# Performance work log

Hardware: AMD Instinct MI355X
Metric: run time of the kernel (lower is better)

The kernel has to match this reference:

```python
import jax, jax.numpy as jnp
import numpy as np
import math

B, T, C, H = 2, 2048, 512, 8
K, DIL = 3, 1
EPS = 1e-5


def _ln(x, g, b):
    m = jnp.mean(x, axis=-1, keepdims=True)
    v = jnp.mean(jnp.square(x - m), axis=-1, keepdims=True)
    return (x - m) * jax.lax.rsqrt(v + EPS) * g + b


def setup_inputs() -> dict:
    key = jax.random.key(0)
    ks = jax.random.split(key, 12)
    s = 0.02
    return {
        "x": jax.random.normal(ks[0], (B, T, C), jnp.float32),
        "conv_w": jax.random.normal(ks[1], (C, C, K), jnp.float32) * s,  # OIH
        "conv_b": jax.random.normal(ks[2], (C,), jnp.float32) * s,
        "g1": jnp.ones((C,), jnp.float32), "b1": jnp.zeros((C,), jnp.float32),
        "qkv_w": jax.random.normal(ks[3], (C, 3 * C), jnp.float32) * s,
        "qkv_b": jax.random.normal(ks[4], (3 * C,), jnp.float32) * s,
        "proj_w": jax.random.normal(ks[5], (C, C), jnp.float32) * s,
        "proj_b": jax.random.normal(ks[6], (C,), jnp.float32) * s,
        "g2": jnp.ones((C,), jnp.float32), "b2": jnp.zeros((C,), jnp.float32),
        "ffn_w1": jax.random.normal(ks[7], (C, 2 * C), jnp.float32) * s,
        "ffn_b1": jax.random.normal(ks[8], (2 * C,), jnp.float32) * s,
        "ffn_w2": jax.random.normal(ks[9], (2 * C, C), jnp.float32) * s,
        "ffn_b2": jax.random.normal(ks[10], (C,), jnp.float32) * s,
        "g3": jnp.ones((C,), jnp.float32), "b3": jnp.zeros((C,), jnp.float32),
    }


def reference(x, conv_w, conv_b, g1, b1, qkv_w, qkv_b, proj_w, proj_b,
              g2, b2, ffn_w1, ffn_b1, ffn_w2, ffn_b2, g3, b3):
    b, t, c = x.shape
    hd = c // H
    # --- causal dilated conv (left-pad only == pad both + right-trim) ---
    pad = (K - 1) * DIL
    xc = jnp.transpose(x, (0, 2, 1))  # [B,C,T]
    conv = jax.lax.conv_general_dilated(
        xc, conv_w, window_strides=(1,), padding=[(pad, 0)],
        rhs_dilation=(DIL,), dimension_numbers=("NCH", "OIH", "NCH"))
    conv = conv + conv_b[None, :, None]
    x = _ln(x + jnp.transpose(conv, (0, 2, 1)), g1, b1)
    # --- causal self-attention ---
    qkv = (x @ qkv_w + qkv_b).reshape(b, t, 3, H, hd)
    qkv = jnp.transpose(qkv, (2, 0, 3, 1, 4))  # [3,B,H,T,hd]
    q, k, v = qkv[0], qkv[1], qkv[2]
    scores = jnp.einsum("bhqd,bhkd->bhqk", q, k) / math.sqrt(hd)
    causal = jnp.tril(jnp.ones((t, t), bool))
    scores = jnp.where(causal, scores, -jnp.inf)
    attn = jax.nn.softmax(scores, axis=-1)
    out = jnp.einsum("bhqk,bhkd->bhqd", attn, v)
    out = jnp.transpose(out, (0, 2, 1, 3)).reshape(b, t, c)
    out = out @ proj_w + proj_b
    x = _ln(x + out, g2, b2)
    # --- FFN ---
    ffn = jax.nn.relu(x @ ffn_w1 + ffn_b1) @ ffn_w2 + ffn_b2
    return _ln(x + ffn, g3, b3)
```

## Files before the change

### kernel.cpp

```cpp
#include <hip/hip_runtime.h>
#include <hip/hip_bf16.h>

#define TT 2048

typedef __attribute__((ext_vector_type(4))) float f32x4;
typedef __attribute__((ext_vector_type(8))) __bf16 bf16x8;
typedef __attribute__((ext_vector_type(4))) short short4v;

enum { M_CONV = 0, M_QKV = 1, M_PROJ = 2, M_FFN1 = 3, M_FFN2 = 4 };

__device__ __forceinline__ void gload16(const void* g, void* l) {
    __builtin_amdgcn_global_load_lds(
        (__attribute__((address_space(1))) void*)g,
        (__attribute__((address_space(3))) void*)l, 16, 0, 0);
}

__device__ __forceinline__ short f2bf(float f) {
    unsigned u = __float_as_uint(f);
    u = (u + 0x7fffu + ((u >> 16) & 1u)) >> 16;
    return (short)u;
}

__global__ void cast_all(const float* __restrict__ conv_w, const float* __restrict__ x,
                         short* __restrict__ cwT, short* __restrict__ xpad) {
    int idx = blockIdx.x * 256 + threadIdx.x;
    if (idx < 786432) {
        int tap = idx >> 18, i = (idx >> 9) & 511, o = idx & 511;
        cwT[(size_t)o * 1536 + tap * 512 + i] = f2bf(conv_w[((size_t)o * 512 + i) * 3 + tap]);
        return;
    }
    idx -= 786432;
    if (idx < 2099200) {
        int i = idx & 511, rp = idx >> 9;
        int bb = rp / 2050, rr = rp - bb * 2050;
        int t = rr - 2;
        float v = (t >= 0) ? x[((size_t)(bb << 11) + t) * 512 + i] : 0.f;
        xpad[((size_t)bb * 2050 + rr) * 512 + i] = f2bf(v);
    }
}

__global__ __launch_bounds__(256) void transpose_cast(
    const float* __restrict__ qkv_w, const float* __restrict__ proj_w,
    const float* __restrict__ f1w, const float* __restrict__ f2w,
    short* __restrict__ qkvT, short* __restrict__ projT,
    short* __restrict__ f1T, short* __restrict__ f2T) {
    int t = blockIdx.x;
    const float* src; short* dst; int K, N, lt;
    if (t < 768)       { src = qkv_w;  dst = qkvT;  K = 512;  N = 1536; lt = t; }
    else if (t < 1024) { src = proj_w; dst = projT; K = 512;  N = 512;  lt = t - 768; }
    else if (t < 1536) { src = f1w;    dst = f1T;   K = 512;  N = 1024; lt = t - 1024; }
    else               { src = f2w;    dst = f2T;   K = 1024; N = 512;  lt = t - 1536; }
    int ntn = N >> 5;
    int kt = lt / ntn, nt = lt - kt * ntn;
    int k0 = kt * 32, n0 = nt * 32;
    __shared__ float tile[32][33];
    int c = threadIdx.x & 31, r = threadIdx.x >> 5;
    #pragma unroll
    for (int i = 0; i < 4; i++)
        tile[r + i * 8][c] = src[(size_t)(k0 + r + i * 8) * N + n0 + c];
    __syncthreads();
    #pragma unroll
    for (int i = 0; i < 4; i++)
        dst[(size_t)(n0 + r + i * 8) * K + k0 + c] = f2bf(tile[c][r + i * 8]);
}

__global__ __launch_bounds__(512) void ln_row(const float* __restrict__ in,
                                              const float* __restrict__ g,
                                              const float* __restrict__ b,
                                              float* __restrict__ outf,
                                              short* __restrict__ outb) {
    int row = blockIdx.x * 8 + (threadIdx.x >> 6);
    int l = threadIdx.x & 63;
    const float* p = in + (size_t)row * 512 + l * 8;
    f32x4 v0 = *(const f32x4*)p;
    f32x4 v1 = *(const f32x4*)(p + 4);
    float s = 0.f, ss = 0.f;
    #pragma unroll
    for (int i = 0; i < 4; i++) { s += v0[i]; ss += v0[i] * v0[i]; }
    #pragma unroll
    for (int i = 0; i < 4; i++) { s += v1[i]; ss += v1[i] * v1[i]; }
    #pragma unroll
    for (int off = 1; off < 64; off <<= 1) {
        s  += __shfl_xor(s, off);
        ss += __shfl_xor(ss, off);
    }
    float mean = s * (1.f / 512);
    float var  = ss * (1.f / 512) - mean * mean;
    float rstd = rsqrtf(var + 1e-5f);
    f32x4 g0 = *(const f32x4*)(g + l * 8), g1 = *(const f32x4*)(g + l * 8 + 4);
    f32x4 b0 = *(const f32x4*)(b + l * 8), b1 = *(const f32x4*)(b + l * 8 + 4);
    f32x4 o0, o1;
    #pragma unroll
    for (int i = 0; i < 4; i++) {
        o0[i] = (v0[i] - mean) * rstd * g0[i] + b0[i];
        o1[i] = (v1[i] - mean) * rstd * g1[i] + b1[i];
    }
    float* q = outf + (size_t)row * 512 + l * 8;
    *(f32x4*)q = o0;
    *(f32x4*)(q + 4) = o1;
    if (outb) {
        short4v p0, p1;
        #pragma unroll
        for (int i = 0; i < 4; i++) { p0[i] = f2bf(o0[i]); p1[i] = f2bf(o1[i]); }
        *(short4v*)(outb + (size_t)row * 512 + l * 8) = p0;
        *(short4v*)(outb + (size_t)row * 512 + l * 8 + 4) = p1;
    }
}

template<int MODE>
__device__ __forceinline__ const short* a_ptr(const short* A, int m0, int r, int kk, int K) {
    if constexpr (MODE == M_CONV) {
        int row = m0 + r;
        int bb = row >> 11, t5 = row & 2047;
        int tap = kk >> 9, k2 = kk & 511;
        return A + ((size_t)(bb * 2050 + t5 + tap) * 512 + k2);
    } else {
        return A + ((size_t)(m0 + r) * K + kk);
    }
}

template<int MODE>
__global__ __launch_bounds__(256) void gemm_mfma(
    const short* __restrict__ A, const short* __restrict__ Bw,
    const float* __restrict__ bias, const float* __restrict__ res,
    void* __restrict__ Cout, short* __restrict__ vTb, int K) {
    __shared__ short As[64 * 64];
    __shared__ short Bs[64 * 64];
    const int tid = threadIdx.x;
    const int w = tid >> 6, l = tid & 63;
    const int wm = w >> 1, wn = w & 1;
    const int lr = l & 15, lc = l >> 4;
    const int m0 = blockIdx.x * 64, n0 = blockIdx.y * 64;
    f32x4 acc[2][2];
    #pragma unroll
    for (int mf = 0; mf < 2; mf++)
        #pragma unroll
        for (int nf = 0; nf < 2; nf++) acc[mf][nf] = (f32x4){0.f, 0.f, 0.f, 0.f};

    for (int k0 = 0; k0 < K; k0 += 64) {
        #pragma unroll
        for (int i = 0; i < 2; i++) {
            int u = i * 256 + tid;
            int r = u >> 3, c = (u & 7) ^ (r & 7);
            gload16(a_ptr<MODE>(A, m0, r, k0 + c * 8, K), (char*)As + u * 16);
            gload16(Bw + ((size_t)(n0 + r) * K + k0 + c * 8), (char*)Bs + u * 16);
        }
        __syncthreads();
        bf16x8 af[2][2], bfv[2][2];
        #pragma unroll
        for (int mf = 0; mf < 2; mf++)
            #pragma unroll
            for (int ks = 0; ks < 2; ks++) {
                int rr = wm * 32 + mf * 16 + lr;
                int cc = (ks * 4 + lc) ^ (rr & 7);
                af[mf][ks] = *(const bf16x8*)&As[rr * 64 + cc * 8];
            }
        #pragma unroll
        for (int nf = 0; nf < 2; nf++)
            #pragma unroll
            for (int ks = 0; ks < 2; ks++) {
                int rr = wn * 32 + nf * 16 + lr;
                int cc = (ks * 4 + lc) ^ (rr & 7);
                bfv[nf][ks] = *(const bf16x8*)&Bs[rr * 64 + cc * 8];
            }
        __builtin_amdgcn_s_setprio(1);
        #pragma unroll
        for (int nf = 0; nf < 2; nf++)
            #pragma unroll
            for (int ks = 0; ks < 2; ks++)
                #pragma unroll
                for (int mf = 0; mf < 2; mf++)
                    acc[mf][nf] = __builtin_amdgcn_mfma_f32_16x16x32_bf16(
                        af[mf][ks], bfv[nf][ks], acc[mf][nf], 0, 0, 0);
        __builtin_amdgcn_s_setprio(0);
        __syncthreads();
    }
    #pragma unroll
    for (int mf = 0; mf < 2; mf++) {
        int row0 = m0 + wm * 32 + mf * 16 + lc * 4;
        #pragma unroll
        for (int nf = 0; nf < 2; nf++) {
            int col = n0 + wn * 32 + nf * 16 + lr;
            float bv = bias[col];
            if constexpr (MODE == M_CONV || MODE == M_PROJ || MODE == M_FFN2) {
                float* Cf = (float*)Cout;
                #pragma unroll
                for (int rg = 0; rg < 4; rg++) {
                    size_t off = (size_t)(row0 + rg) * 512 + col;
                    Cf[off] = acc[mf][nf][rg] + bv + res[off];
                }
            } else if constexpr (MODE == M_FFN1) {
                short* Cb = (short*)Cout;
                #pragma unroll
                for (int rg = 0; rg < 4; rg++)
                    Cb[(size_t)(row0 + rg) * 1024 + col] =
                        f2bf(fmaxf(acc[mf][nf][rg] + bv, 0.f));
            } else {
                short* Cb = (short*)Cout;
                float v[4];
                #pragma unroll
                for (int rg = 0; rg < 4; rg++) {
                    v[rg] = acc[mf][nf][rg] + bv;
                    Cb[(size_t)(row0 + rg) * 1536 + col] = f2bf(v[rg]);
                }
                if (col >= 1024) {
                    int vc = col - 1024, hh = vc >> 6, dd = vc & 63;
                    int bb = row0 >> 11, t5 = row0 & 2047;
                    short4v pk = {f2bf(v[0]), f2bf(v[1]), f2bf(v[2]), f2bf(v[3])};
                    *(short4v*)&vTb[((size_t)((bb << 3) + hh) * 64 + dd) * 2048 + t5] = pk;
                }
            }
        }
    }
}

__global__ __launch_bounds__(512) void attn_mfma(const short* __restrict__ qkvb,
                                                 const short* __restrict__ vTb,
                                                 short* __restrict__ aout) {
    __shared__ short SM[25600];
    __shared__ float Mm[4][16], Lm[4][16];
    const int tid = threadIdx.x;
    const int w = tid >> 6, l = tid & 63;
    const int half = w >> 2, wq = w & 3;
    const int lr = l & 15, lc = l >> 4;
    const int L = blockIdx.x;
    const int bh = L & 15;
    const int qt = 31 - (L >> 4);
    const int b = bh >> 3, h = bh & 7;
    const int qr = wq * 16, q0 = qt * 64;
    const int pbase = 16384 + w * (16 * 72);

    {
        int u = tid, r = u >> 3, c = (u & 7) ^ (r & 7);
        gload16(qkvb + ((size_t)(b * 2048 + q0 + r) * 1536 + h * 64 + c * 8),
                (char*)&SM[16384] + u * 16);
    }
    __syncthreads();
    bf16x8 aq[2];
    #pragma unroll
    for (int ks = 0; ks < 2; ks++) {
        int rr = qr + lr;
        int cc = (lc + 4 * ks) ^ (rr & 7);
        aq[ks] = *(const bf16x8*)&SM[16384 + rr * 64 + cc * 8];
    }
    __syncthreads();

    f32x4 o[4];
    float mst[4], lst[4];
    #pragma unroll
    for (int nf = 0; nf < 4; nf++) o[nf] = (f32x4){0.f, 0.f, 0.f, 0.f};
    #pragma unroll
    for (int rg = 0; rg < 4; rg++) { mst[rg] = -1e30f; lst[rg] = 0.f; }

    const int NS = (qt + 2) >> 1;
    for (int ss = 0; ss < NS; ss++) {
        const int kt0 = 2 * ss, kt1 = 2 * ss + 1;
        {
            int u = tid, r = u >> 3, c = (u & 7) ^ (r & 7);
            gload16(qkvb + ((size_t)(b * 2048 + kt0 * 64 + r) * 1536 + 512 + h * 64 + c * 8),
                    (char*)&SM[0] + u * 16);
            gload16(vTb + ((size_t)(bh * 64 + r) * 2048 + kt0 * 64 + c * 8),
                    (char*)&SM[8192] + u * 16);
            if (kt1 <= qt) {
                gload16(qkvb + ((size_t)(b * 2048 + kt1 * 64 + r) * 1536 + 512 + h * 64 + c * 8),
                        (char*)&SM[4096] + u * 16);
                gload16(vTb + ((size_t)(bh * 64 + r) * 2048 + kt1 * 64 + c * 8),
                        (char*)&SM[12288] + u * 16);
            }
        }
        __syncthreads();
        const int mykt = 2 * ss + half;
        if (mykt <= qt) {
            const int kofs = half * 4096;
            const int vofs = 8192 + half * 4096;
            f32x4 s[4];
            #pragma unroll
            for (int nf = 0; nf < 4; nf++) s[nf] = (f32x4){0.f, 0.f, 0.f, 0.f};
            __builtin_amdgcn_s_setprio(1);
            #pragma unroll
            for (int nf = 0; nf < 4; nf++) {
                #pragma unroll
                for (int ks = 0; ks < 2; ks++) {
                    int rr = nf * 16 + lr;
                    int cc = (lc + 4 * ks) ^ (rr & 7);
                    bf16x8 bk = *(const bf16x8*)&SM[kofs + rr * 64 + cc * 8];
                    s[nf] = __builtin_amdgcn_mfma_f32_16x16x32_bf16(aq[ks], bk, s[nf], 0, 0, 0);
                }
            }
            __builtin_amdgcn_s_setprio(0);
            const bool diag = (mykt == qt);
            #pragma unroll
            for (int nf = 0; nf < 4; nf++) {
                #pragma unroll
                for (int rg = 0; rg < 4; rg++) {
                    float v = s[nf][rg] * 0.125f;
                    if (diag && (nf * 16 + lr > qr + lc * 4 + rg)) v = -1e30f;
                    s[nf][rg] = v;
                }
            }
            float rm[4];
            int ok = 1;
            #pragma unroll
            for (int rg = 0; rg < 4; rg++) {
                float m_ = fmaxf(fmaxf(s[0][rg], s[1][rg]), fmaxf(s[2][rg], s[3][rg]));
                m_ = fmaxf(m_, __shfl_xor(m_, 1));
                m_ = fmaxf(m_, __shfl_xor(m_, 2));
                m_ = fmaxf(m_, __shfl_xor(m_, 4));
                m_ = fmaxf(m_, __shfl_xor(m_, 8));
                rm[rg] = m_;
                ok &= (m_ <= mst[rg] + 8.f);
            }
            if (!__all(ok)) {
                #pragma unroll
                for (int rg = 0; rg < 4; rg++) {
                    float mn = fmaxf(mst[rg], rm[rg]);
                    float alpha = __expf(mst[rg] - mn);
                    mst[rg] = mn;
                    lst[rg] *= alpha;
                    #pragma unroll
                    for (int nf = 0; nf < 4; nf++) o[nf][rg] *= alpha;
                }
            }
            #pragma unroll
            for (int rg = 0; rg < 4; rg++) {
                float p0 = __expf(s[0][rg] - mst[rg]);
                float p1 = __expf(s[1][rg] - mst[rg]);
                float p2 = __expf(s[2][rg] - mst[rg]);
                float p3 = __expf(s[3][rg] - mst[rg]);
                int prow = pbase + (lc * 4 + rg) * 72;
                SM[prow      + lr] = f2bf(p0);
                SM[prow + 16 + lr] = f2bf(p1);
                SM[prow + 32 + lr] = f2bf(p2);
                SM[prow + 48 + lr] = f2bf(p3);
                float rs = p0 + p1 + p2 + p3;
                rs += __shfl_xor(rs, 1);
                rs += __shfl_xor(rs, 2);
                rs += __shfl_xor(rs, 4);
                rs += __shfl_xor(rs, 8);
                lst[rg] += rs;
            }
            bf16x8 pa[2];
            #pragma unroll
            for (int ks = 0; ks < 2; ks++)
                pa[ks] = *(const bf16x8*)&SM[pbase + lr * 72 + ks * 32 + lc * 8];
            __builtin_amdgcn_s_setprio(1);
            #pragma unroll
            for (int nf = 0; nf < 4; nf++) {
                #pragma unroll
                for (int ks = 0; ks < 2; ks++) {
                    int rr = nf * 16 + lr;
                    int cc = (lc + 4 * ks) ^ (rr & 7);
                    bf16x8 bv = *(const bf16x8*)&SM[vofs + rr * 64 + cc * 8];
                    o[nf] = __builtin_amdgcn_mfma_f32_16x16x32_bf16(pa[ks], bv, o[nf], 0, 0, 0);
                }
            }
            __builtin_amdgcn_s_setprio(0);
        }
        __syncthreads();
    }

    float* Osm = (float*)&SM[16384];
    if (half == 1) {
        #pragma unroll
        for (int rg = 0; rg < 4; rg++) {
            int row = lc * 4 + rg;
            if (lr == 0) { Mm[wq][row] = mst[rg]; Lm[wq][row] = lst[rg]; }
            #pragma unroll
            for (int nf = 0; nf < 4; nf++)
                Osm[(wq * 16 + row) * 68 + nf * 16 + lr] = o[nf][rg];
        }
    }
    __syncthreads();
    if (half == 0) {
        #pragma unroll
        for (int rg = 0; rg < 4; rg++) {
            int row = lc * 4 + rg;
            float m2 = Mm[wq][row], l2 = Lm[wq][row];
            float mn = fmaxf(mst[rg], m2);
            float a1 = __expf(mst[rg] - mn);
            float a2 = __expf(m2 - mn);
            float lm = lst[rg] * a1 + l2 * a2;
            float inv = 1.f / lm;
            #pragma unroll
            for (int nf = 0; nf < 4; nf++) {
                float ov = (o[nf][rg] * a1 + Osm[(wq * 16 + row) * 68 + nf * 16 + lr] * a2) * inv;
                aout[(size_t)(b * 2048 + q0 + qr + row) * 512 + h * 64 + nf * 16 + lr] =
                    f2bf(ov);
            }
        }
    }
}

extern "C" void kernel_launch(void* const* d_in, const int* in_sizes, int n_in,
                              void* d_out, int out_size, void* d_ws, size_t ws_size,
                              hipStream_t stream) {
    const float* x      = (const float*)d_in[0];
    const float* conv_w = (const float*)d_in[1];
    const float* conv_b = (const float*)d_in[2];
    const float* g1     = (const float*)d_in[3];
    const float* b1     = (const float*)d_in[4];
    const float* qkv_w  = (const float*)d_in[5];
    const float* qkv_b  = (const float*)d_in[6];
    const float* proj_w = (const float*)d_in[7];
    const float* proj_b = (const float*)d_in[8];
    const float* g2     = (const float*)d_in[9];
    const float* b2     = (const float*)d_in[10];
    const float* ffn_w1 = (const float*)d_in[11];
    const float* ffn_b1 = (const float*)d_in[12];
    const float* ffn_w2 = (const float*)d_in[13];
    const float* ffn_b2 = (const float*)d_in[14];
    const float* g3     = (const float*)d_in[15];
    const float* b3     = (const float*)d_in[16];
    float* out = (float*)d_out;

    char* p = (char*)d_ws;
    short* cwT   = (short*)p;  p += 786432 * 2;
    short* qkvT  = (short*)p;  p += 786432 * 2;
    short* projT = (short*)p;  p += 262144 * 2;
    short* f1T   = (short*)p;  p += 524288 * 2;
    short* f2T   = (short*)p;  p += 524288 * 2;
    short* xpad  = (short*)p;  p += 2099200 * 2;
    float* yb    = (float*)p;  p += 2097152 * 4;
    float* x1f   = (float*)p;  p += 2097152 * 4;
    short* x1b   = (short*)p;  p += 2097152 * 2;
    short* qkvb  = (short*)p;  p += 6291456 * 2;
    short* vTb   = (short*)p;  p += 2097152 * 2;
    float* x2f     = x1f;
    short* x2b     = x1b;
    short* attnout = xpad;
    short* hb      = qkvb;

    cast_all<<<11272, 256, 0, stream>>>(conv_w, x, cwT, xpad);
    transpose_cast<<<2048, 256, 0, stream>>>(qkv_w, proj_w, ffn_w1, ffn_w2,
                                             qkvT, projT, f1T, f2T);
    gemm_mfma<M_CONV><<<dim3(64, 8), 256, 0, stream>>>(
        xpad, cwT, conv_b, x, yb, nullptr, 1536);
    ln_row<<<512, 512, 0, stream>>>(yb, g1, b1, x1f, x1b);
    gemm_mfma<M_QKV><<<dim3(64, 24), 256, 0, stream>>>(
        x1b, qkvT, qkv_b, nullptr, qkvb, vTb, 512);
    attn_mfma<<<512, 512, 0, stream>>>(qkvb, vTb, attnout);
    gemm_mfma<M_PROJ><<<dim3(64, 8), 256, 0, stream>>>(
        attnout, projT, proj_b, x1f, yb, nullptr, 512);
    ln_row<<<512, 512, 0, stream>>>(yb, g2, b2, x2f, x2b);
    gemm_mfma<M_FFN1><<<dim3(64, 16), 256, 0, stream>>>(
        x2b, f1T, ffn_b1, nullptr, hb, nullptr, 512);
    gemm_mfma<M_FFN2><<<dim3(64, 8), 256, 0, stream>>>(
        hb, f2T, ffn_b2, x2f, yb, nullptr, 1024);
    ln_row<<<512, 512, 0, stream>>>(yb, g3, b3, out, nullptr);
}
```

Before: 144.8 us.

## Double-buffer K tiles in attention, load V to registers, shrink GEMM blocks, merge prep kernels

```diff
diff --git a/kernel.cpp b/kernel.cpp
--- a/kernel.cpp
+++ b/kernel.cpp
@@ -21,9 +21,35 @@
     return (short)u;
 }
 
-__global__ void cast_all(const float* __restrict__ conv_w, const float* __restrict__ x,
-                         short* __restrict__ cwT, short* __restrict__ xpad) {
-    int idx = blockIdx.x * 256 + threadIdx.x;
+__global__ __launch_bounds__(256) void prep_all(
+    const float* __restrict__ conv_w, const float* __restrict__ x,
+    const float* __restrict__ qkv_w, const float* __restrict__ proj_w,
+    const float* __restrict__ f1w, const float* __restrict__ f2w,
+    short* __restrict__ cwT, short* __restrict__ xpad,
+    short* __restrict__ qkvT, short* __restrict__ projT,
+    short* __restrict__ f1T, short* __restrict__ f2T) {
+    if (blockIdx.x < 2048) {
+        int t = blockIdx.x;
+        const float* src; short* dst; int K, N, lt;
+        if (t < 768)       { src = qkv_w;  dst = qkvT;  K = 512;  N = 1536; lt = t; }
+        else if (t < 1024) { src = proj_w; dst = projT; K = 512;  N = 512;  lt = t - 768; }
+        else if (t < 1536) { src = f1w;    dst = f1T;   K = 512;  N = 1024; lt = t - 1024; }
+        else               { src = f2w;    dst = f2T;   K = 1024; N = 512;  lt = t - 1536; }
+        int ntn = N >> 5;
+        int kt = lt / ntn, nt = lt - kt * ntn;
+        int k0 = kt * 32, n0 = nt * 32;
+        __shared__ float tile[32][33];
+        int c = threadIdx.x & 31, r = threadIdx.x >> 5;
+        #pragma unroll
+        for (int i = 0; i < 4; i++)
+            tile[r + i * 8][c] = src[(size_t)(k0 + r + i * 8) * N + n0 + c];
+        __syncthreads();
+        #pragma unroll
+        for (int i = 0; i < 4; i++)
+            dst[(size_t)(n0 + r + i * 8) * K + k0 + c] = f2bf(tile[c][r + i * 8]);
+        return;
+    }
+    int idx = (blockIdx.x - 2048) * 256 + threadIdx.x;
     if (idx < 786432) {
         int tap = idx >> 18, i = (idx >> 9) & 511, o = idx & 511;
         cwT[(size_t)o * 1536 + tap * 512 + i] = f2bf(conv_w[((size_t)o * 512 + i) * 3 + tap]);
@@ -37,31 +63,6 @@
         float v = (t >= 0) ? x[((size_t)(bb << 11) + t) * 512 + i] : 0.f;
         xpad[((size_t)bb * 2050 + rr) * 512 + i] = f2bf(v);
     }
-}
-
-__global__ __launch_bounds__(256) void transpose_cast(
-    const float* __restrict__ qkv_w, const float* __restrict__ proj_w,
-    const float* __restrict__ f1w, const float* __restrict__ f2w,
-    short* __restrict__ qkvT, short* __restrict__ projT,
-    short* __restrict__ f1T, short* __restrict__ f2T) {
-    int t = blockIdx.x;
-    const float* src; short* dst; int K, N, lt;
-    if (t < 768)       { src = qkv_w;  dst = qkvT;  K = 512;  N = 1536; lt = t; }
-    else if (t < 1024) { src = proj_w; dst = projT; K = 512;  N = 512;  lt = t - 768; }
-    else if (t < 1536) { src = f1w;    dst = f1T;   K = 512;  N = 1024; lt = t - 1024; }
-    else               { src = f2w;    dst = f2T;   K = 1024; N = 512;  lt = t - 1536; }
-    int ntn = N >> 5;
-    int kt = lt / ntn, nt = lt - kt * ntn;
-    int k0 = kt * 32, n0 = nt * 32;
-    __shared__ float tile[32][33];
-    int c = threadIdx.x & 31, r = threadIdx.x >> 5;
-    #pragma unroll
-    for (int i = 0; i < 4; i++)
-        tile[r + i * 8][c] = src[(size_t)(k0 + r + i * 8) * N + n0 + c];
-    __syncthreads();
-    #pragma unroll
-    for (int i = 0; i < 4; i++)
-        dst[(size_t)(n0 + r + i * 8) * K + k0 + c] = f2bf(tile[c][r + i * 8]);
 }
 
 __global__ __launch_bounds__(512) void ln_row(const float* __restrict__ in,
@@ -120,7 +121,7 @@
 }
 
 template<int MODE>
-__global__ __launch_bounds__(256) void gemm_mfma(
+__global__ __launch_bounds__(128) void gemm_mfma(
     const short* __restrict__ A, const short* __restrict__ Bw,
     const float* __restrict__ bias, const float* __restrict__ res,
     void* __restrict__ Cout, short* __restrict__ vTb, int K) {
@@ -128,44 +129,43 @@
     __shared__ short Bs[64 * 64];
     const int tid = threadIdx.x;
     const int w = tid >> 6, l = tid & 63;
-    const int wm = w >> 1, wn = w & 1;
     const int lr = l & 15, lc = l >> 4;
     const int m0 = blockIdx.x * 64, n0 = blockIdx.y * 64;
-    f32x4 acc[2][2];
+    f32x4 acc[2][4];
     #pragma unroll
     for (int mf = 0; mf < 2; mf++)
         #pragma unroll
-        for (int nf = 0; nf < 2; nf++) acc[mf][nf] = (f32x4){0.f, 0.f, 0.f, 0.f};
+        for (int nf = 0; nf < 4; nf++) acc[mf][nf] = (f32x4){0.f, 0.f, 0.f, 0.f};
 
     for (int k0 = 0; k0 < K; k0 += 64) {
         #pragma unroll
-        for (int i = 0; i < 2; i++) {
-            int u = i * 256 + tid;
+        for (int i = 0; i < 4; i++) {
+            int u = i * 128 + tid;
             int r = u >> 3, c = (u & 7) ^ (r & 7);
             gload16(a_ptr<MODE>(A, m0, r, k0 + c * 8, K), (char*)As + u * 16);
             gload16(Bw + ((size_t)(n0 + r) * K + k0 + c * 8), (char*)Bs + u * 16);
         }
         __syncthreads();
-        bf16x8 af[2][2], bfv[2][2];
+        bf16x8 af[2][2], bfv[4][2];
         #pragma unroll
         for (int mf = 0; mf < 2; mf++)
             #pragma unroll
             for (int ks = 0; ks < 2; ks++) {
-                int rr = wm * 32 + mf * 16 + lr;
+                int rr = w * 32 + mf * 16 + lr;
                 int cc = (ks * 4 + lc) ^ (rr & 7);
                 af[mf][ks] = *(const bf16x8*)&As[rr * 64 + cc * 8];
             }
         #pragma unroll
-        for (int nf = 0; nf < 2; nf++)
+        for (int nf = 0; nf < 4; nf++)
             #pragma unroll
             for (int ks = 0; ks < 2; ks++) {
-                int rr = wn * 32 + nf * 16 + lr;
+                int rr = nf * 16 + lr;
                 int cc = (ks * 4 + lc) ^ (rr & 7);
                 bfv[nf][ks] = *(const bf16x8*)&Bs[rr * 64 + cc * 8];
             }
         __builtin_amdgcn_s_setprio(1);
         #pragma unroll
-        for (int nf = 0; nf < 2; nf++)
+        for (int nf = 0; nf < 4; nf++)
             #pragma unroll
             for (int ks = 0; ks < 2; ks++)
                 #pragma unroll
@@ -177,10 +177,10 @@
     }
     #pragma unroll
     for (int mf = 0; mf < 2; mf++) {
-        int row0 = m0 + wm * 32 + mf * 16 + lc * 4;
-        #pragma unroll
-        for (int nf = 0; nf < 2; nf++) {
-            int col = n0 + wn * 32 + nf * 16 + lr;
+        int row0 = m0 + w * 32 + mf * 16 + lc * 4;
+        #pragma unroll
+        for (int nf = 0; nf < 4; nf++) {
+            int col = n0 + nf * 16 + lr;
             float bv = bias[col];
             if constexpr (MODE == M_CONV || MODE == M_PROJ || MODE == M_FFN2) {
                 float* Cf = (float*)Cout;
@@ -234,6 +234,11 @@
         int u = tid, r = u >> 3, c = (u & 7) ^ (r & 7);
         gload16(qkvb + ((size_t)(b * 2048 + q0 + r) * 1536 + h * 64 + c * 8),
                 (char*)&SM[16384] + u * 16);
+        gload16(qkvb + ((size_t)(b * 2048 + r) * 1536 + 512 + h * 64 + c * 8),
+                (char*)&SM[0] + u * 16);
+        if (qt >= 1)
+            gload16(qkvb + ((size_t)(b * 2048 + 64 + r) * 1536 + 512 + h * 64 + c * 8),
+                    (char*)&SM[4096] + u * 16);
     }
     __syncthreads();
     bf16x8 aq[2];
@@ -254,25 +259,28 @@
 
     const int NS = (qt + 2) >> 1;
     for (int ss = 0; ss < NS; ss++) {
-        const int kt0 = 2 * ss, kt1 = 2 * ss + 1;
-        {
+        const int mykt = 2 * ss + half;
+        const int kofs = (ss & 1) * 8192 + half * 4096;
+        bf16x8 vf[4][2];
+        if (mykt <= qt) {
+            #pragma unroll
+            for (int nf = 0; nf < 4; nf++)
+                #pragma unroll
+                for (int ks = 0; ks < 2; ks++)
+                    vf[nf][ks] = *(const bf16x8*)(vTb +
+                        (size_t)(bh * 64 + nf * 16 + lr) * 2048 + mykt * 64 + (lc + 4 * ks) * 8);
+        }
+        if (ss + 1 < NS) {
+            int nb = ((ss + 1) & 1) * 8192;
+            int ktA = 2 * (ss + 1);
             int u = tid, r = u >> 3, c = (u & 7) ^ (r & 7);
-            gload16(qkvb + ((size_t)(b * 2048 + kt0 * 64 + r) * 1536 + 512 + h * 64 + c * 8),
-                    (char*)&SM[0] + u * 16);
-            gload16(vTb + ((size_t)(bh * 64 + r) * 2048 + kt0 * 64 + c * 8),
-                    (char*)&SM[8192] + u * 16);
-            if (kt1 <= qt) {
-                gload16(qkvb + ((size_t)(b * 2048 + kt1 * 64 + r) * 1536 + 512 + h * 64 + c * 8),
-                        (char*)&SM[4096] + u * 16);
-                gload16(vTb + ((size_t)(bh * 64 + r) * 2048 + kt1 * 64 + c * 8),
-                        (char*)&SM[12288] + u * 16);
-            }
-        }
-        __syncthreads();
-        const int mykt = 2 * ss + half;
+            gload16(qkvb + ((size_t)(b * 2048 + ktA * 64 + r) * 1536 + 512 + h * 64 + c * 8),
+                    (char*)&SM[nb] + u * 16);
+            if (ktA + 1 <= qt)
+                gload16(qkvb + ((size_t)(b * 2048 + (ktA + 1) * 64 + r) * 1536 + 512 + h * 64 + c * 8),
+                        (char*)&SM[nb + 4096] + u * 16);
+        }
         if (mykt <= qt) {
-            const int kofs = half * 4096;
-            const int vofs = 8192 + half * 4096;
             f32x4 s[4];
             #pragma unroll
             for (int nf = 0; nf < 4; nf++) s[nf] = (f32x4){0.f, 0.f, 0.f, 0.f};
@@ -345,15 +353,10 @@
                 pa[ks] = *(const bf16x8*)&SM[pbase + lr * 72 + ks * 32 + lc * 8];
             __builtin_amdgcn_s_setprio(1);
             #pragma unroll
-            for (int nf = 0; nf < 4; nf++) {
-                #pragma unroll
-                for (int ks = 0; ks < 2; ks++) {
-                    int rr = nf * 16 + lr;
-                    int cc = (lc + 4 * ks) ^ (rr & 7);
-                    bf16x8 bv = *(const bf16x8*)&SM[vofs + rr * 64 + cc * 8];
-                    o[nf] = __builtin_amdgcn_mfma_f32_16x16x32_bf16(pa[ks], bv, o[nf], 0, 0, 0);
-                }
-            }
+            for (int nf = 0; nf < 4; nf++)
+                #pragma unroll
+                for (int ks = 0; ks < 2; ks++)
+                    o[nf] = __builtin_amdgcn_mfma_f32_16x16x32_bf16(pa[ks], vf[nf][ks], o[nf], 0, 0, 0);
             __builtin_amdgcn_s_setprio(0);
         }
         __syncthreads();
@@ -430,21 +433,20 @@
     short* attnout = xpad;
     short* hb      = qkvb;
 
-    cast_all<<<11272, 256, 0, stream>>>(conv_w, x, cwT, xpad);
-    transpose_cast<<<2048, 256, 0, stream>>>(qkv_w, proj_w, ffn_w1, ffn_w2,
-                                             qkvT, projT, f1T, f2T);
-    gemm_mfma<M_CONV><<<dim3(64, 8), 256, 0, stream>>>(
+    prep_all<<<13320, 256, 0, stream>>>(conv_w, x, qkv_w, proj_w, ffn_w1, ffn_w2,
+                                        cwT, xpad, qkvT, projT, f1T, f2T);
+    gemm_mfma<M_CONV><<<dim3(64, 8), 128, 0, stream>>>(
         xpad, cwT, conv_b, x, yb, nullptr, 1536);
     ln_row<<<512, 512, 0, stream>>>(yb, g1, b1, x1f, x1b);
-    gemm_mfma<M_QKV><<<dim3(64, 24), 256, 0, stream>>>(
+    gemm_mfma<M_QKV><<<dim3(64, 24), 128, 0, stream>>>(
         x1b, qkvT, qkv_b, nullptr, qkvb, vTb, 512);
     attn_mfma<<<512, 512, 0, stream>>>(qkvb, vTb, attnout);
-    gemm_mfma<M_PROJ><<<dim3(64, 8), 256, 0, stream>>>(
+    gemm_mfma<M_PROJ><<<dim3(64, 8), 128, 0, stream>>>(
         attnout, projT, proj_b, x1f, yb, nullptr, 512);
     ln_row<<<512, 512, 0, stream>>>(yb, g2, b2, x2f, x2b);
-    gemm_mfma<M_FFN1><<<dim3(64, 16), 256, 0, stream>>>(
+    gemm_mfma<M_FFN1><<<dim3(64, 16), 128, 0, stream>>>(
         x2b, f1T, ffn_b1, nullptr, hb, nullptr, 512);
-    gemm_mfma<M_FFN2><<<dim3(64, 8), 256, 0, stream>>>(
+    gemm_mfma<M_FFN2><<<dim3(64, 8), 128, 0, stream>>>(
         hb, f2T, ffn_b2, x2f, yb, nullptr, 1024);
     ln_row<<<512, 512, 0, stream>>>(yb, g3, b3, out, nullptr);
 }
```

After: 155.9 us. 1.08x slower.
